# Performance work log

Measured on AMD Instinct MI355X. Metric: run time of the kernel, lower is better.

## Reference

```python
import jax, jax.numpy as jnp
import numpy as np

B, S, E = 32, 577, 1024
H = 16
D = E // H  # head_size = 64


def setup_inputs() -> dict:
    key = jax.random.key(0)
    ks = jax.random.split(key, 5)
    scale_init = E ** -0.5
    x = jax.random.normal(ks[0], (B, S, E), dtype=jnp.float32)
    # Per-head projection weights. torch Linear weight is [out,in]; we store
    # [H, E, D] so that x @ Wq[h] == torch_linear(x) with weight Wq[h].T.
    Wq = jax.random.normal(ks[1], (H, E, D), dtype=jnp.float32) * scale_init
    Wk = jax.random.normal(ks[2], (H, E, D), dtype=jnp.float32) * scale_init
    Wv = jax.random.normal(ks[3], (H, E, D), dtype=jnp.float32) * scale_init
    # Output projection (with bias, as in nn.Linear default)
    Wo = jax.random.normal(ks[4], (E, E), dtype=jnp.float32) * scale_init
    bo = jnp.zeros((E,), dtype=jnp.float32)
    return {"x": x, "Wq": Wq, "Wk": Wk, "Wv": Wv, "Wo": Wo, "bo": bo}


def reference(x, Wq, Wk, Wv, Wo, bo):
    scale = D ** -0.5
    # Per-head QKV projections, vectorized over heads: [B,H,S,D]
    q = jnp.einsum('bse,hed->bhsd', x, Wq)
    k = jnp.einsum('bse,hed->bhsd', x, Wk)
    v = jnp.einsum('bse,hed->bhsd', x, Wv)
    scores = jnp.einsum('bhsd,bhtd->bhst', q, k) * scale  # [B,H,S,S]
    attn = jax.nn.softmax(scores, axis=-1)
    out = jnp.einsum('bhst,bhtd->bhsd', attn, v)  # [B,H,S,D]
    # Concat heads: head h occupies slice [h*D:(h+1)*D], matching torch.cat order
    out = out.transpose(0, 2, 1, 3).reshape(B, S, E)
    return out @ Wo.T + bo  # torch Linear: x @ W.T + b
```

## Files before the change

kernel.cpp:

```cpp
#include <hip/hip_runtime.h>
#include <hip/hip_bf16.h>
#include <stdint.h>

using sh8   = __attribute__((ext_vector_type(8))) short;
using f32x4 = __attribute__((ext_vector_type(4))) float;

#define MFMA16(a, b, c) __builtin_amdgcn_mfma_f32_16x16x32_bf16(a, b, c, 0, 0, 0)
#define EXP2F(x) __builtin_amdgcn_exp2f(x)

static constexpr int BB = 32, SS = 577, HH = 16;
static constexpr int MM = BB * SS;
static constexpr int SPAD = 640;
static constexpr float QSCALE = 0.18033688011112042f;

__device__ __forceinline__ ushort f2b(float f) {
  union { float f; uint32_t u; } v{f};
  uint32_t r = v.u + 0x7FFFu + ((v.u >> 16) & 1u);
  return (ushort)(r >> 16);
}

#if __has_builtin(__builtin_amdgcn_cvt_pk_bf16_f32)
typedef __attribute__((ext_vector_type(2))) __bf16 bf16x2_t;
__device__ __forceinline__ uint32_t pk_bf16(float a, float b) {
  union { bf16x2_t v; uint32_t u; } c;
  c.v = __builtin_amdgcn_cvt_pk_bf16_f32(a, b);
  return c.u;
}
#else
__device__ __forceinline__ uint32_t pk_bf16(float a, float b) {
  return (uint32_t)f2b(a) | ((uint32_t)f2b(b) << 16);
}
#endif

__device__ __forceinline__ void gld16(const ushort* g, ushort* l) {
  __builtin_amdgcn_global_load_lds(
      (const __attribute__((address_space(1))) uint32_t*)g,
      (__attribute__((address_space(3))) uint32_t*)l, 16, 0, 0);
}

__global__ __launch_bounds__(256)
void convert_f32_bf16_v4(const float* __restrict__ in, ushort* __restrict__ out, int n4) {
  int i = blockIdx.x * 256 + threadIdx.x;
  const int stride = gridDim.x * 256;
  for (; i < n4; i += stride) {
    const float4 f = ((const float4*)in)[i];
    ushort4 u;
    u.x = f2b(f.x); u.y = f2b(f.y); u.z = f2b(f.z); u.w = f2b(f.w);
    ((ushort4*)out)[i] = u;
  }
}

__global__ __launch_bounds__(256)
void convert_wqkv(const float* __restrict__ Wq, const float* __restrict__ Wk,
                  const float* __restrict__ Wv, ushort* __restrict__ Wt) {
  __shared__ ushort T[64 * 72];
  const int tid = threadIdx.x;
  const int kt = blockIdx.x, sh = blockIdx.y;
  const int sel = sh >> 4, h = sh & 15;
  const float* W = (sel == 0) ? Wq : ((sel == 1) ? Wk : Wv);
  const float qs = (sel == 0) ? QSCALE : 1.0f;
  const int rr = tid >> 4;
  const int rc = (tid & 15) * 4;
#pragma unroll
  for (int p = 0; p < 64; p += 16) {
    const float4 f = *(const float4*)(W + (size_t)h * 65536 + (size_t)(kt * 64 + p + rr) * 64 + rc);
    ushort4 u;
    u.x = f2b(f.x * qs); u.y = f2b(f.y * qs); u.z = f2b(f.z * qs); u.w = f2b(f.w * qs);
    *(ushort4*)&T[(p + rr) * 72 + rc] = u;
  }
  __syncthreads();
  const int dd = tid >> 2;
  const int c16 = (tid & 3) * 16;
  sh8 v0, v1;
#pragma unroll
  for (int j = 0; j < 8; j++) v0[j] = (short)T[(c16 + j) * 72 + dd];
#pragma unroll
  for (int j = 0; j < 8; j++) v1[j] = (short)T[(c16 + 8 + j) * 72 + dd];
  ushort* op = Wt + ((size_t)sel * 1024 + h * 64 + dd) * 1024 + kt * 64 + c16;
  *(sh8*)op = v0;
  *(sh8*)(op + 8) = v1;
}

template <int MODE>
__global__ __launch_bounds__(256)
void gemm_bt(const ushort* __restrict__ A, const ushort* __restrict__ Bt,
             ushort* __restrict__ Cb, float* __restrict__ Cf,
             const float* __restrict__ bias, int M, int N, int K) {
  __shared__ ushort Al[128 * 32];
  __shared__ ushort Bl[128 * 32];
  const int tid = threadIdx.x;
  const int lane = tid & 63, w = tid >> 6;
  const int l15 = lane & 15, quad = lane >> 4;
  const int wm = (w >> 1) * 64, wn = (w & 1) * 64;
  const int m0 = blockIdx.y * 128, n0 = blockIdx.x * 128;

  f32x4 acc[4][4];
#pragma unroll
  for (int i = 0; i < 4; i++)
#pragma unroll
    for (int j = 0; j < 4; j++) acc[i][j] = f32x4{0.f, 0.f, 0.f, 0.f};

  const int u0 = w * 128 + lane;
  const int u1 = u0 + 64;
  const int ar0 = u0 >> 2, ac0 = (u0 & 3) * 8;
  const int ar1 = u1 >> 2, ac1 = (u1 & 3) * 8;
  const ushort* ApA0 = A + (size_t)min(m0 + ar0, M - 1) * K + ac0;
  const ushort* ApA1 = A + (size_t)min(m0 + ar1, M - 1) * K + ac1;
  const ushort* BpB0 = Bt + (size_t)(n0 + ar0) * K + ac0;
  const ushort* BpB1 = Bt + (size_t)(n0 + ar1) * K + ac1;
  ushort* lA0 = &Al[u0 * 8];
  ushort* lA1 = &Al[u1 * 8];
  ushort* lB0 = &Bl[u0 * 8];
  ushort* lB1 = &Bl[u1 * 8];

  for (int k0 = 0; k0 < K; k0 += 32) {
    __syncthreads();
    gld16(ApA0 + k0, lA0);
    gld16(ApA1 + k0, lA1);
    gld16(BpB0 + k0, lB0);
    gld16(BpB1 + k0, lB1);
    __syncthreads();
    sh8 af[4], bf[4];
#pragma unroll
    for (int i = 0; i < 4; i++) af[i] = *(const sh8*)&Al[(wm + i * 16 + l15) * 32 + quad * 8];
#pragma unroll
    for (int j = 0; j < 4; j++) bf[j] = *(const sh8*)&Bl[(wn + j * 16 + l15) * 32 + quad * 8];
#pragma unroll
    for (int i = 0; i < 4; i++)
#pragma unroll
      for (int j = 0; j < 4; j++) acc[i][j] = MFMA16(bf[j], af[i], acc[i][j]);
  }

#pragma unroll
  for (int i = 0; i < 4; i++) {
    const int row = m0 + wm + i * 16 + l15;
    const bool ok = row < M;
#pragma unroll
    for (int j = 0; j < 4; j++) {
      const int col0 = n0 + wn + j * 16 + quad * 4;
      if (MODE == 0) {
        uint2 pk;
        pk.x = pk_bf16(acc[i][j][0], acc[i][j][1]);
        pk.y = pk_bf16(acc[i][j][2], acc[i][j][3]);
        if (ok) *(uint2*)&Cb[(size_t)row * N + col0] = pk;
      } else {
        const float4 b4 = *(const float4*)&bias[col0];
        float4 v;
        v.x = acc[i][j][0] + b4.x; v.y = acc[i][j][1] + b4.y;
        v.z = acc[i][j][2] + b4.z; v.w = acc[i][j][3] + b4.w;
        if (ok) *(float4*)&Cf[(size_t)row * N + col0] = v;
      }
    }
  }
}

__global__ __launch_bounds__(256)
void transpose_v(const ushort* __restrict__ QKV, ushort* __restrict__ Vtg) {
  __shared__ ushort T[64 * 72];
  const int tid = threadIdx.x;
  const int st = blockIdx.x, bh = blockIdx.y;
  const int b = bh >> 4, h = bh & 15;
  const int sr = tid >> 3;
  const int sc = (tid & 7) * 8;
#pragma unroll
  for (int p = 0; p < 64; p += 32) {
    const int s = st * 64 + p + sr;
    uint4 d = uint4{0u, 0u, 0u, 0u};
    if (s < SS) d = *(const uint4*)(QKV + ((size_t)b * SS + s) * 3072 + 2048 + h * 64 + sc);
    *(uint4*)&T[(p + sr) * 72 + sc] = d;
  }
  __syncthreads();
  const int dd = tid >> 2;
  const int s16 = (tid & 3) * 16;
  sh8 v0, v1;
#pragma unroll
  for (int j = 0; j < 8; j++) v0[j] = (short)T[(s16 + j) * 72 + dd];
#pragma unroll
  for (int j = 0; j < 8; j++) v1[j] = (short)T[(s16 + 8 + j) * 72 + dd];
  ushort* outp = Vtg + ((size_t)bh * 64 + dd) * SPAD + st * 64 + s16;
  *(sh8*)outp = v0;
  *(sh8*)(outp + 8) = v1;
}

__global__ __launch_bounds__(256)
void flash_attn(const ushort* __restrict__ QKV, const ushort* __restrict__ Vtg,
                ushort* __restrict__ Ob) {
  __shared__ ushort Kl[64 * 72];
  __shared__ ushort Vl[64 * 72];
  __shared__ ushort Pl[64 * 72];
  const int tid = threadIdx.x;
  const int lane = tid & 63, w = tid >> 6;
  const int l15 = lane & 15, quad = lane >> 4;
  const int qb = blockIdx.x, bh = blockIdx.y;
  const int b = bh >> 4, h = bh & 15;

  const int qr = qb * 64 + w * 16 + l15;
  const int qrc = min(qr, SS - 1);
  const ushort* qrow = QKV + ((size_t)b * SS + qrc) * 3072 + h * 64;
  const sh8 qf0 = *(const sh8*)(qrow + quad * 8);
  const sh8 qf1 = *(const sh8*)(qrow + 32 + quad * 8);

  sh8 ones;
#pragma unroll
  for (int j = 0; j < 8; j++) ones[j] = (short)0x3F80;

  f32x4 o[4];
  f32x4 acc_l = f32x4{0.f, 0.f, 0.f, 0.f};
#pragma unroll
  for (int t = 0; t < 4; t++) o[t] = f32x4{0.f, 0.f, 0.f, 0.f};

  const int sr = tid >> 3;
  const int sc = (tid & 7) * 8;
  const ushort* Kbase = QKV + ((size_t)b * SS) * 3072 + 1024 + h * 64 + sc;
  const ushort* Vb0 = Vtg + ((size_t)bh * 64 + sr) * SPAD + sc;
  const ushort* Vb1 = Vtg + ((size_t)bh * 64 + 32 + sr) * SPAD + sc;
  ushort* plw = &Pl[(w * 16 + l15) * 72];

  for (int kt = 0; kt < 10; kt++) {
    const int kb = kt * 64;
    const int kp0 = min(kb + sr, SS - 1);
    const int kp1 = min(kb + 32 + sr, SS - 1);
    const uint4 kd0 = *(const uint4*)(Kbase + (size_t)kp0 * 3072);
    const uint4 kd1 = *(const uint4*)(Kbase + (size_t)kp1 * 3072);
    const uint4 vd0 = *(const uint4*)(Vb0 + kb);
    const uint4 vd1 = *(const uint4*)(Vb1 + kb);
    __syncthreads();
    *(uint4*)&Kl[sr * 72 + sc] = kd0;
    *(uint4*)&Kl[(32 + sr) * 72 + sc] = kd1;
    *(uint4*)&Vl[sr * 72 + sc] = vd0;
    *(uint4*)&Vl[(32 + sr) * 72 + sc] = vd1;
    __syncthreads();

#pragma unroll
    for (int tn = 0; tn < 4; tn++) {
      f32x4 s = f32x4{0.f, 0.f, 0.f, 0.f};
      const sh8 k0 = *(const sh8*)&Kl[(tn * 16 + l15) * 72 + quad * 8];
      const sh8 k1 = *(const sh8*)&Kl[(tn * 16 + l15) * 72 + 32 + quad * 8];
      s = MFMA16(k0, qf0, s);
      s = MFMA16(k1, qf1, s);
      if (kt == 9) {
#pragma unroll
        for (int r = 0; r < 4; r++)
          if ((tn * 16 + quad * 4 + r) != 0) s[r] = -1e30f;
      }
      uint2 pp;
      pp.x = pk_bf16(EXP2F(s[0]), EXP2F(s[1]));
      pp.y = pk_bf16(EXP2F(s[2]), EXP2F(s[3]));
      *(uint2*)(plw + tn * 16 + quad * 4) = pp;
    }
    const sh8 pa0 = *(const sh8*)(plw + quad * 8);
    const sh8 pa1 = *(const sh8*)(plw + 32 + quad * 8);
    acc_l = MFMA16(ones, pa0, acc_l);
    acc_l = MFMA16(ones, pa1, acc_l);
#pragma unroll
    for (int t = 0; t < 4; t++) {
      const sh8 v0 = *(const sh8*)&Vl[(t * 16 + l15) * 72 + quad * 8];
      const sh8 v1 = *(const sh8*)&Vl[(t * 16 + l15) * 72 + 32 + quad * 8];
      o[t] = MFMA16(v0, pa0, o[t]);
      o[t] = MFMA16(v1, pa1, o[t]);
    }
  }

  const float inv = 1.0f / acc_l[0];
  const int s = qb * 64 + w * 16 + l15;
  if (s < SS) {
    ushort* op = Ob + ((size_t)b * SS + s) * 1024 + h * 64 + quad * 4;
#pragma unroll
    for (int t = 0; t < 4; t++) {
      uint2 ov;
      ov.x = pk_bf16(o[t][0] * inv, o[t][1] * inv);
      ov.y = pk_bf16(o[t][2] * inv, o[t][3] * inv);
      *(uint2*)(op + t * 16) = ov;
    }
  }
}

extern "C" void kernel_launch(void* const* d_in, const int* in_sizes, int n_in,
                              void* d_out, int out_size, void* d_ws, size_t ws_size,
                              hipStream_t stream) {
  const float* x  = (const float*)d_in[0];
  const float* Wq = (const float*)d_in[1];
  const float* Wk = (const float*)d_in[2];
  const float* Wv = (const float*)d_in[3];
  const float* Wo = (const float*)d_in[4];
  const float* bo = (const float*)d_in[5];
  float* out = (float*)d_out;

  ushort* Xb  = (ushort*)d_ws;
  ushort* Wt  = Xb  + (size_t)MM * 1024;
  ushort* Wob = Wt  + (size_t)3072 * 1024;
  ushort* QKV = Wob + (size_t)1024 * 1024;
  ushort* Vtg = QKV + (size_t)MM * 3072;
  ushort* Ob  = Xb;

  convert_f32_bf16_v4<<<4096, 256, 0, stream>>>(x, Xb, MM * 1024 / 4);
  convert_wqkv<<<dim3(16, 48), 256, 0, stream>>>(Wq, Wk, Wv, Wt);
  convert_f32_bf16_v4<<<1024, 256, 0, stream>>>(Wo, Wob, 1024 * 1024 / 4);
  gemm_bt<0><<<dim3(24, 145), 256, 0, stream>>>(Xb, Wt, QKV, nullptr, nullptr, MM, 3072, 1024);
  transpose_v<<<dim3(10, 512), 256, 0, stream>>>(QKV, Vtg);
  flash_attn<<<dim3(10, 512), 256, 0, stream>>>(QKV, Vtg, Ob);
  gemm_bt<1><<<dim3(8, 145), 256, 0, stream>>>(Ob, Wob, nullptr, out, bo, MM, 1024, 1024);
}
```

Measured before the change: 493.3 us.

## Deepen GEMM K-tile with XOR swizzle; double query rows per flash-attention block

The GEMM now stages 64-wide K slices through LDS using an XOR-swizzled layout, so it runs half as many barrier-separated iterations and avoids LDS bank conflicts without padding. Flash attention now handles 128 query rows per block (two 16-row groups per wave). This reuses each K/V tile for twice as many queries and halves the number of blocks. K and V loads also switch to direct global-to-LDS copies with the same swizzle. In exchange it uses more LDS and registers per block, which may lower occupancy.

Result: faster. 456.6 us (-7.4%).

```diff
diff --git a/kernel.cpp b/kernel.cpp
--- a/kernel.cpp
+++ b/kernel.cpp
@@ -86,8 +86,8 @@
 void gemm_bt(const ushort* __restrict__ A, const ushort* __restrict__ Bt,
              ushort* __restrict__ Cb, float* __restrict__ Cf,
              const float* __restrict__ bias, int M, int N, int K) {
-  __shared__ ushort Al[128 * 32];
-  __shared__ ushort Bl[128 * 32];
+  __shared__ ushort Al[128 * 64];
+  __shared__ ushort Bl[128 * 64];
   const int tid = threadIdx.x;
   const int lane = tid & 63, w = tid >> 6;
   const int l15 = lane & 15, quad = lane >> 4;
@@ -100,35 +100,43 @@
 #pragma unroll
     for (int j = 0; j < 4; j++) acc[i][j] = f32x4{0.f, 0.f, 0.f, 0.f};
 
-  const int u0 = w * 128 + lane;
-  const int u1 = u0 + 64;
-  const int ar0 = u0 >> 2, ac0 = (u0 & 3) * 8;
-  const int ar1 = u1 >> 2, ac1 = (u1 & 3) * 8;
-  const ushort* ApA0 = A + (size_t)min(m0 + ar0, M - 1) * K + ac0;
-  const ushort* ApA1 = A + (size_t)min(m0 + ar1, M - 1) * K + ac1;
-  const ushort* BpB0 = Bt + (size_t)(n0 + ar0) * K + ac0;
-  const ushort* BpB1 = Bt + (size_t)(n0 + ar1) * K + ac1;
-  ushort* lA0 = &Al[u0 * 8];
-  ushort* lA1 = &Al[u1 * 8];
-  ushort* lB0 = &Bl[u0 * 8];
-  ushort* lB1 = &Bl[u1 * 8];
-
-  for (int k0 = 0; k0 < K; k0 += 32) {
+  const int rbase = tid >> 3;
+  const int swzc = ((tid & 7) ^ (rbase & 7)) * 8;
+  const ushort* Ag[4]; const ushort* Bg[4];
+  ushort* lA[4]; ushort* lB[4];
+#pragma unroll
+  for (int i = 0; i < 4; i++) {
+    const int r = i * 32 + rbase;
+    Ag[i] = A + (size_t)min(m0 + r, M - 1) * K + swzc;
+    Bg[i] = Bt + (size_t)(n0 + r) * K + swzc;
+    lA[i] = &Al[(i * 256 + tid) * 8];
+    lB[i] = &Bl[(i * 256 + tid) * 8];
+  }
+  const int swz = l15 & 7;
+  const int ck0 = (quad ^ swz) * 8;
+  const int ck1 = ((quad + 4) ^ swz) * 8;
+
+  for (int k0 = 0; k0 < K; k0 += 64) {
     __syncthreads();
-    gld16(ApA0 + k0, lA0);
-    gld16(ApA1 + k0, lA1);
-    gld16(BpB0 + k0, lB0);
-    gld16(BpB1 + k0, lB1);
+#pragma unroll
+    for (int i = 0; i < 4; i++) {
+      gld16(Ag[i] + k0, lA[i]);
+      gld16(Bg[i] + k0, lB[i]);
+    }
     __syncthreads();
-    sh8 af[4], bf[4];
-#pragma unroll
-    for (int i = 0; i < 4; i++) af[i] = *(const sh8*)&Al[(wm + i * 16 + l15) * 32 + quad * 8];
-#pragma unroll
-    for (int j = 0; j < 4; j++) bf[j] = *(const sh8*)&Bl[(wn + j * 16 + l15) * 32 + quad * 8];
-#pragma unroll
-    for (int i = 0; i < 4; i++)
-#pragma unroll
-      for (int j = 0; j < 4; j++) acc[i][j] = MFMA16(bf[j], af[i], acc[i][j]);
+#pragma unroll
+    for (int kk = 0; kk < 2; kk++) {
+      const int ck = kk ? ck1 : ck0;
+      sh8 af[4], bf[4];
+#pragma unroll
+      for (int i = 0; i < 4; i++) af[i] = *(const sh8*)&Al[(wm + i * 16 + l15) * 64 + ck];
+#pragma unroll
+      for (int j = 0; j < 4; j++) bf[j] = *(const sh8*)&Bl[(wn + j * 16 + l15) * 64 + ck];
+#pragma unroll
+      for (int i = 0; i < 4; i++)
+#pragma unroll
+        for (int j = 0; j < 4; j++) acc[i][j] = MFMA16(bf[j], af[i], acc[i][j]);
+    }
   }
 
 #pragma unroll
@@ -185,92 +193,116 @@
 __global__ __launch_bounds__(256)
 void flash_attn(const ushort* __restrict__ QKV, const ushort* __restrict__ Vtg,
                 ushort* __restrict__ Ob) {
-  __shared__ ushort Kl[64 * 72];
-  __shared__ ushort Vl[64 * 72];
-  __shared__ ushort Pl[64 * 72];
+  __shared__ ushort Kl[64 * 64];
+  __shared__ ushort Vl[64 * 64];
+  __shared__ ushort Pl[128 * 72];
   const int tid = threadIdx.x;
   const int lane = tid & 63, w = tid >> 6;
   const int l15 = lane & 15, quad = lane >> 4;
   const int qb = blockIdx.x, bh = blockIdx.y;
   const int b = bh >> 4, h = bh & 15;
 
-  const int qr = qb * 64 + w * 16 + l15;
-  const int qrc = min(qr, SS - 1);
-  const ushort* qrow = QKV + ((size_t)b * SS + qrc) * 3072 + h * 64;
-  const sh8 qf0 = *(const sh8*)(qrow + quad * 8);
-  const sh8 qf1 = *(const sh8*)(qrow + 32 + quad * 8);
+  sh8 qf[2][2];
+#pragma unroll
+  for (int g = 0; g < 2; g++) {
+    const int qr = qb * 128 + w * 32 + g * 16 + l15;
+    const ushort* qrow = QKV + ((size_t)b * SS + min(qr, SS - 1)) * 3072 + h * 64;
+    qf[g][0] = *(const sh8*)(qrow + quad * 8);
+    qf[g][1] = *(const sh8*)(qrow + 32 + quad * 8);
+  }
 
   sh8 ones;
 #pragma unroll
   for (int j = 0; j < 8; j++) ones[j] = (short)0x3F80;
 
-  f32x4 o[4];
-  f32x4 acc_l = f32x4{0.f, 0.f, 0.f, 0.f};
-#pragma unroll
-  for (int t = 0; t < 4; t++) o[t] = f32x4{0.f, 0.f, 0.f, 0.f};
-
-  const int sr = tid >> 3;
-  const int sc = (tid & 7) * 8;
-  const ushort* Kbase = QKV + ((size_t)b * SS) * 3072 + 1024 + h * 64 + sc;
-  const ushort* Vb0 = Vtg + ((size_t)bh * 64 + sr) * SPAD + sc;
-  const ushort* Vb1 = Vtg + ((size_t)bh * 64 + 32 + sr) * SPAD + sc;
-  ushort* plw = &Pl[(w * 16 + l15) * 72];
+  f32x4 o[2][4];
+  f32x4 acc_l[2];
+#pragma unroll
+  for (int g = 0; g < 2; g++) {
+    acc_l[g] = f32x4{0.f, 0.f, 0.f, 0.f};
+#pragma unroll
+    for (int t = 0; t < 4; t++) o[g][t] = f32x4{0.f, 0.f, 0.f, 0.f};
+  }
+
+  const int r0 = tid >> 3;
+  const int swzs = ((tid & 7) ^ (r0 & 7)) * 8;
+  const ushort* Kg = QKV + (size_t)b * SS * 3072 + 1024 + h * 64 + swzs;
+  const ushort* Vg0 = Vtg + ((size_t)bh * 64 + r0) * SPAD + swzs;
+  const ushort* Vg1 = Vtg + ((size_t)bh * 64 + 32 + r0) * SPAD + swzs;
+  ushort* lK0 = &Kl[tid * 8];
+  ushort* lK1 = &Kl[(256 + tid) * 8];
+  ushort* lV0 = &Vl[tid * 8];
+  ushort* lV1 = &Vl[(256 + tid) * 8];
+
+  const int swz = l15 & 7;
+  const int ca0 = (quad ^ swz) * 8;
+  const int ca1 = ((quad + 4) ^ swz) * 8;
+  ushort* plw[2] = { &Pl[(w * 32 + l15) * 72], &Pl[(w * 32 + 16 + l15) * 72] };
 
   for (int kt = 0; kt < 10; kt++) {
     const int kb = kt * 64;
-    const int kp0 = min(kb + sr, SS - 1);
-    const int kp1 = min(kb + 32 + sr, SS - 1);
-    const uint4 kd0 = *(const uint4*)(Kbase + (size_t)kp0 * 3072);
-    const uint4 kd1 = *(const uint4*)(Kbase + (size_t)kp1 * 3072);
-    const uint4 vd0 = *(const uint4*)(Vb0 + kb);
-    const uint4 vd1 = *(const uint4*)(Vb1 + kb);
     __syncthreads();
-    *(uint4*)&Kl[sr * 72 + sc] = kd0;
-    *(uint4*)&Kl[(32 + sr) * 72 + sc] = kd1;
-    *(uint4*)&Vl[sr * 72 + sc] = vd0;
-    *(uint4*)&Vl[(32 + sr) * 72 + sc] = vd1;
+    gld16(Kg + (size_t)min(kb + r0, SS - 1) * 3072, lK0);
+    gld16(Kg + (size_t)min(kb + 32 + r0, SS - 1) * 3072, lK1);
+    gld16(Vg0 + kb, lV0);
+    gld16(Vg1 + kb, lV1);
     __syncthreads();
 
 #pragma unroll
     for (int tn = 0; tn < 4; tn++) {
-      f32x4 s = f32x4{0.f, 0.f, 0.f, 0.f};
-      const sh8 k0 = *(const sh8*)&Kl[(tn * 16 + l15) * 72 + quad * 8];
-      const sh8 k1 = *(const sh8*)&Kl[(tn * 16 + l15) * 72 + 32 + quad * 8];
-      s = MFMA16(k0, qf0, s);
-      s = MFMA16(k1, qf1, s);
-      if (kt == 9) {
-#pragma unroll
-        for (int r = 0; r < 4; r++)
-          if ((tn * 16 + quad * 4 + r) != 0) s[r] = -1e30f;
+      const int kr = tn * 16 + l15;
+      const sh8 k0 = *(const sh8*)&Kl[kr * 64 + ca0];
+      const sh8 k1 = *(const sh8*)&Kl[kr * 64 + ca1];
+#pragma unroll
+      for (int g = 0; g < 2; g++) {
+        f32x4 s = f32x4{0.f, 0.f, 0.f, 0.f};
+        s = MFMA16(k0, qf[g][0], s);
+        s = MFMA16(k1, qf[g][1], s);
+        if (kt == 9) {
+#pragma unroll
+          for (int r = 0; r < 4; r++)
+            if ((tn * 16 + quad * 4 + r) != 0) s[r] = -1e30f;
+        }
+        uint2 pp;
+        pp.x = pk_bf16(EXP2F(s[0]), EXP2F(s[1]));
+        pp.y = pk_bf16(EXP2F(s[2]), EXP2F(s[3]));
+        *(uint2*)(plw[g] + tn * 16 + quad * 4) = pp;
       }
-      uint2 pp;
-      pp.x = pk_bf16(EXP2F(s[0]), EXP2F(s[1]));
-      pp.y = pk_bf16(EXP2F(s[2]), EXP2F(s[3]));
-      *(uint2*)(plw + tn * 16 + quad * 4) = pp;
-    }
-    const sh8 pa0 = *(const sh8*)(plw + quad * 8);
-    const sh8 pa1 = *(const sh8*)(plw + 32 + quad * 8);
-    acc_l = MFMA16(ones, pa0, acc_l);
-    acc_l = MFMA16(ones, pa1, acc_l);
+    }
+    sh8 pa[2][2];
+#pragma unroll
+    for (int g = 0; g < 2; g++) {
+      pa[g][0] = *(const sh8*)(plw[g] + quad * 8);
+      pa[g][1] = *(const sh8*)(plw[g] + 32 + quad * 8);
+      acc_l[g] = MFMA16(ones, pa[g][0], acc_l[g]);
+      acc_l[g] = MFMA16(ones, pa[g][1], acc_l[g]);
+    }
 #pragma unroll
     for (int t = 0; t < 4; t++) {
-      const sh8 v0 = *(const sh8*)&Vl[(t * 16 + l15) * 72 + quad * 8];
-      const sh8 v1 = *(const sh8*)&Vl[(t * 16 + l15) * 72 + 32 + quad * 8];
-      o[t] = MFMA16(v0, pa0, o[t]);
-      o[t] = MFMA16(v1, pa1, o[t]);
-    }
-  }
-
-  const float inv = 1.0f / acc_l[0];
-  const int s = qb * 64 + w * 16 + l15;
-  if (s < SS) {
-    ushort* op = Ob + ((size_t)b * SS + s) * 1024 + h * 64 + quad * 4;
-#pragma unroll
-    for (int t = 0; t < 4; t++) {
-      uint2 ov;
-      ov.x = pk_bf16(o[t][0] * inv, o[t][1] * inv);
-      ov.y = pk_bf16(o[t][2] * inv, o[t][3] * inv);
-      *(uint2*)(op + t * 16) = ov;
+      const int vr = t * 16 + l15;
+      const sh8 v0 = *(const sh8*)&Vl[vr * 64 + ca0];
+      const sh8 v1 = *(const sh8*)&Vl[vr * 64 + ca1];
+#pragma unroll
+      for (int g = 0; g < 2; g++) {
+        o[g][t] = MFMA16(v0, pa[g][0], o[g][t]);
+        o[g][t] = MFMA16(v1, pa[g][1], o[g][t]);
+      }
+    }
+  }
+
+#pragma unroll
+  for (int g = 0; g < 2; g++) {
+    const float inv = 1.0f / acc_l[g][0];
+    const int s = qb * 128 + w * 32 + g * 16 + l15;
+    if (s < SS) {
+      ushort* op = Ob + ((size_t)b * SS + s) * 1024 + h * 64 + quad * 4;
+#pragma unroll
+      for (int t = 0; t < 4; t++) {
+        uint2 ov;
+        ov.x = pk_bf16(o[g][t][0] * inv, o[g][t][1] * inv);
+        ov.y = pk_bf16(o[g][t][2] * inv, o[g][t][3] * inv);
+        *(uint2*)(op + t * 16) = ov;
+      }
     }
   }
 }
@@ -298,6 +330,6 @@
   convert_f32_bf16_v4<<<1024, 256, 0, stream>>>(Wo, Wob, 1024 * 1024 / 4);
   gemm_bt<0><<<dim3(24, 145), 256, 0, stream>>>(Xb, Wt, QKV, nullptr, nullptr, MM, 3072, 1024);
   transpose_v<<<dim3(10, 512), 256, 0, stream>>>(QKV, Vtg);
-  flash_attn<<<dim3(10, 512), 256, 0, stream>>>(QKV, Vtg, Ob);
+  flash_attn<<<dim3(5, 512), 256, 0, stream>>>(QKV, Vtg, Ob);
   gemm_bt<1><<<dim3(8, 145), 256, 0, stream>>>(Ob, Wob, nullptr, out, bo, MM, 1024, 1024);
 }
```
